# Kernel tuning notes

Measured on AMD Instinct MI355X. Metric: run time of the kernel, lower is better.

The kernel has to match this reference:

```python
import jax, jax.numpy as jnp
import numpy as np
import math

N, B, T, E = 4, 8, 2, 1024
H, D = 16, 64
S, L = 2048, 1024
NB = N * B

def setup_inputs() -> dict:
    key = jax.random.key(0)
    ks = jax.random.split(key, 10)
    sc = 0.02
    return {
        'hidden_states': jax.random.normal(ks[0], (NB, T, E), jnp.float32),
        'attention_mask': jnp.zeros((NB, 1, 1, S + L + T), jnp.float32),
        'past_prefix_key': jax.random.normal(ks[1], (N, H, S, D), jnp.float32),
        'past_prefix_value': jax.random.normal(ks[2], (N, H, S, D), jnp.float32),
        'past_key': jax.random.normal(ks[3], (NB, H, L, D), jnp.float32),
        'past_value': jax.random.normal(ks[4], (NB, H, L, D), jnp.float32),
        'Wq': jax.random.normal(ks[5], (E, E), jnp.float32) * sc,
        'bq': jnp.zeros((E,), jnp.float32),
        'Wk': jax.random.normal(ks[6], (E, E), jnp.float32) * sc,
        'bk': jnp.zeros((E,), jnp.float32),
        'Wv': jax.random.normal(ks[7], (E, E), jnp.float32) * sc,
        'bv': jnp.zeros((E,), jnp.float32),
    }

def _heads(x):
    # (NB, T, E) -> (NB, H, T, D)
    return x.reshape(NB, T, H, D).transpose(0, 2, 1, 3)

def reference(hidden_states, attention_mask, past_prefix_key, past_prefix_value,
              past_key, past_value, Wq, bq, Wk, bk, Wv, bv):
    scale = 1.0 / math.sqrt(D)
    q = _heads(hidden_states @ Wq.T + bq)   # (NB,H,T,D)
    k_new = _heads(hidden_states @ Wk.T + bk)
    v_new = _heads(hidden_states @ Wv.T + bv)

    # prefix scores: broadcast shared prefix KV across beams
    q_beam = q.reshape(N, B, H, T, D)
    prefix_scores = jnp.einsum('bxhtd,bhsd->bxhts', q_beam, past_prefix_key)
    prefix_scores = prefix_scores.reshape(NB, H, T, S) * scale

    # current KV = cached target prefix + new tokens
    k = jnp.concatenate([past_key, k_new], axis=2)   # (NB,H,L+T,D)
    v = jnp.concatenate([past_value, v_new], axis=2)
    cur_scores = jnp.einsum('bhtd,bhsd->bhts', q, k) * scale

    scores = jnp.concatenate([prefix_scores, cur_scores], axis=-1) + attention_mask
    probs = jax.nn.softmax(scores, axis=-1)          # (NB,H,T,S+L+T)

    prefix_probs = probs[..., :S].reshape(N, B, H, T, S)
    cur_probs = probs[..., S:]
    prefix_ctx = jnp.einsum('bxhts,bhsd->bxhtd', prefix_probs, past_prefix_value)
    prefix_ctx = prefix_ctx.reshape(NB, H, T, D)
    ctx = prefix_ctx + jnp.einsum('bhts,bhsd->bhtd', cur_probs, v)

    # (NB,H,T,D) -> (NB,T,E)
    return ctx.transpose(0, 2, 1, 3).reshape(NB, T, H * D)
```

## Files before the change

### kernel.cpp

```cpp
#include <hip/hip_runtime.h>
#include <hip/hip_bf16.h>

#define NB_  32
#define T_   2
#define E_   1024
#define H_   16
#define D_   64
#define S_   2048
#define L_   1024
#define TOT_ (S_ + L_ + T_)

#define PCH_  16
#define PLEN_ (S_ / PCH_)
#define NT_   8
#define CCH_  8
#define CLEN_ (L_ / CCH_)

#define PFXU_ (4 * H_ * PCH_)
#define CURU_ (NB_ * H_ * CCH_)

#define LOG2E_ 1.4426950408889634f
#define QS_ (0.125f * LOG2E_)

#define GLOAD_LDS16(g, l) __builtin_amdgcn_global_load_lds( \
    (const __attribute__((address_space(1))) void*)(g), \
    (__attribute__((address_space(3))) void*)(l), 16, 0, 0)

#define KEEP4(v) asm volatile("" : "+v"((v).x), "+v"((v).y), "+v"((v).z), "+v"((v).w))
#define KEEPF(a) asm volatile("" : "+v"(a))

__global__ __launch_bounds__(256) void qkv_kernel(
    const float* __restrict__ hidden,
    const float* __restrict__ Wq, const float* __restrict__ bq,
    const float* __restrict__ Wk, const float* __restrict__ bk,
    const float* __restrict__ Wv, const float* __restrict__ bv,
    float* __restrict__ qT,
    float* __restrict__ knew,
    float* __restrict__ vnew)
{
    __shared__ float ldsT[128 * 65];
    __shared__ float wlds[8 * 128];
    const int tid  = threadIdx.x;
    const int wave = tid >> 6;
    const int lane = tid & 63;
    const int eg0  = blockIdx.x * 8;
    const int mat  = eg0 >> 10;
    const int e0   = eg0 & 1023;
    int c0 = wave * 2;
    c0 = __builtin_amdgcn_readfirstlane(c0);

    const float* W    = (mat == 0) ? Wq : (mat == 1) ? Wk : Wv;
    const float* bias = (mat == 0) ? bq : (mat == 1) ? bk : bv;

    float aA0 = 0.f, aB0 = 0.f, aA1 = 0.f, aB1 = 0.f;

    for (int k0 = 0; k0 < 1024; k0 += 128) {
        __syncthreads();
        #pragma unroll
        for (int i = 0; i < 32; i++) {
            int f = i * 256 + tid;
            int r = f >> 7;
            int c = f & 127;
            ldsT[c * 65 + r] = hidden[r * 1024 + k0 + c];
        }
        {
            int wr = tid >> 5;
            int wc = (tid & 31) * 4;
            *reinterpret_cast<float4*>(&wlds[wr * 128 + wc]) =
                *reinterpret_cast<const float4*>(&W[(size_t)(e0 + wr) * 1024 + k0 + wc]);
        }
        __syncthreads();

        for (int kk = 0; kk < 128; kk += 4) {
            float h0 = ldsT[(kk + 0) * 65 + lane];
            float h1 = ldsT[(kk + 1) * 65 + lane];
            float h2 = ldsT[(kk + 2) * 65 + lane];
            float h3 = ldsT[(kk + 3) * 65 + lane];
            float4 w0 = *reinterpret_cast<const float4*>(&wlds[(c0 + 0) * 128 + kk]);
            float4 w1 = *reinterpret_cast<const float4*>(&wlds[(c0 + 1) * 128 + kk]);
            aA0 = fmaf(h0, w0.x, aA0); aA0 = fmaf(h1, w0.y, aA0);
            aB0 = fmaf(h2, w0.z, aB0); aB0 = fmaf(h3, w0.w, aB0);
            aA1 = fmaf(h0, w1.x, aA1); aA1 = fmaf(h1, w1.y, aA1);
            aB1 = fmaf(h2, w1.z, aB1); aB1 = fmaf(h3, w1.w, aB1);
        }
    }

    const int r = lane;
    #pragma unroll
    for (int j = 0; j < 2; j++) {
        int e_in = e0 + c0 + j;
        float val = ((j == 0) ? (aA0 + aB0) : (aA1 + aB1)) + bias[e_in];
        if (mat == 0) {
            qT[e_in * 64 + r] = val;
        } else {
            int nb = r >> 1, t = r & 1, h = e_in >> 6, d = e_in & 63;
            float* dst = (mat == 1) ? knew : vnew;
            dst[((nb * H_ + h) * T_ + t) * D_ + d] = val;
        }
    }
}

__global__ __launch_bounds__(256) void cur_partial_kernel(
    const float* __restrict__ mask,
    const float* __restrict__ pk,
    const float* __restrict__ pv,
    const float* __restrict__ qT,
    const float* __restrict__ knew,
    const float* __restrict__ vnew,
    float* __restrict__ cur_ctx,
    float* __restrict__ cur_l)
{
    __shared__ float smem[2080];
    const int tid = threadIdx.x;

    const int u     = blockIdx.x;
    const int b     = u >> 3;
    const int chunk = u & 7;
    const int nb    = b >> 4;
    const int h     = b & 15;
    const int g     = tid >> 4;
    const int l16   = tid & 15;
    const int d0    = l16 * 4;

    float qf0[4], qf1[4];
    #pragma unroll
    for (int j = 0; j < 4; j++) {
        const float* qb = qT + (h * 64 + d0 + j) * 64 + nb * 2;
        qf0[j] = qb[0] * QS_;
        qf1[j] = qb[1] * QS_;
    }

    const float* pk_b = pk + ((nb * H_ + h) * (size_t)L_) * D_;
    const float* pv_b = pv + ((nb * H_ + h) * (size_t)L_) * D_;
    const float* mrow = mask + nb * TOT_ + S_;
    const int p0 = chunk * CLEN_ + g;

    float mreg[8];
    #pragma unroll
    for (int i = 0; i < 8; i++) mreg[i] = mrow[p0 + i * 16] * LOG2E_;

    float4 kf[8], vf[8];
    #pragma unroll
    for (int i = 0; i < 8; i++) {
        kf[i] = *reinterpret_cast<const float4*>(pk_b + (size_t)(p0 + i * 16) * D_ + d0);
        vf[i] = *reinterpret_cast<const float4*>(pv_b + (size_t)(p0 + i * 16) * D_ + d0);
    }
    #pragma unroll
    for (int i = 0; i < 8; i++) { KEEP4(kf[i]); KEEP4(vf[i]); KEEPF(mreg[i]); }

    float l0 = 0.f, l1 = 0.f;
    float a0[4] = {0.f,0.f,0.f,0.f};
    float a1[4] = {0.f,0.f,0.f,0.f};

    #pragma unroll
    for (int i = 0; i < 8; i++) {
        float s0 = fmaf(qf0[0],kf[i].x, qf0[1]*kf[i].y) + fmaf(qf0[2],kf[i].z, qf0[3]*kf[i].w);
        float s1 = fmaf(qf1[0],kf[i].x, qf1[1]*kf[i].y) + fmaf(qf1[2],kf[i].z, qf1[3]*kf[i].w);
        #pragma unroll
        for (int off = 1; off < 16; off <<= 1) {
            s0 += __shfl_xor(s0, off, 64);
            s1 += __shfl_xor(s1, off, 64);
        }
        float e0 = exp2f(s0 + mreg[i]);
        float e1 = exp2f(s1 + mreg[i]);
        l0 += e0; l1 += e1;
        a0[0] += e0 * vf[i].x; a0[1] += e0 * vf[i].y; a0[2] += e0 * vf[i].z; a0[3] += e0 * vf[i].w;
        a1[0] += e1 * vf[i].x; a1[1] += e1 * vf[i].y; a1[2] += e1 * vf[i].z; a1[3] += e1 * vf[i].w;
    }

    if (chunk == 7 && g < 2) {
        const float* kn_b = knew + (nb * H_ + h) * (T_ * D_);
        const float* vn_b = vnew + (nb * H_ + h) * (T_ * D_);
        float4 kfn = *reinterpret_cast<const float4*>(kn_b + g * D_ + d0);
        float s0 = fmaf(qf0[0],kfn.x, qf0[1]*kfn.y) + fmaf(qf0[2],kfn.z, qf0[3]*kfn.w);
        float s1 = fmaf(qf1[0],kfn.x, qf1[1]*kfn.y) + fmaf(qf1[2],kfn.z, qf1[3]*kfn.w);
        #pragma unroll
        for (int off = 1; off < 16; off <<= 1) {
            s0 += __shfl_xor(s0, off, 64);
            s1 += __shfl_xor(s1, off, 64);
        }
        float mC = mrow[L_ + g] * LOG2E_;
        float e0 = exp2f(s0 + mC);
        float e1 = exp2f(s1 + mC);
        l0 += e0; l1 += e1;
        float4 vfn = *reinterpret_cast<const float4*>(vn_b + g * D_ + d0);
        a0[0] += e0 * vfn.x; a0[1] += e0 * vfn.y; a0[2] += e0 * vfn.z; a0[3] += e0 * vfn.w;
        a1[0] += e1 * vfn.x; a1[1] += e1 * vfn.y; a1[2] += e1 * vfn.z; a1[3] += e1 * vfn.w;
    }

    #pragma unroll
    for (int j = 0; j < 4; j++) {
        smem[g * 128 + d0 + j]      = a0[j];
        smem[g * 128 + 64 + d0 + j] = a1[j];
    }
    if (l16 == 0) { smem[2048 + g * 2] = l0; smem[2048 + g * 2 + 1] = l1; }
    __syncthreads();

    if (tid < 128) {
        int t = tid >> 6, d = tid & 63;
        float s = 0.f, l = 0.f;
        for (int g2 = 0; g2 < 16; g2++) {
            s += smem[g2 * 128 + t * 64 + d];
            l += smem[2048 + g2 * 2 + t];
        }
        cur_ctx[(u * 2 + t) * 64 + d] = s;
        if (d == 0) cur_l[u * 2 + t] = l;
    }
}

__global__ __launch_bounds__(256) void pfx_partial_kernel(
    const float* __restrict__ mask,
    const float* __restrict__ pfx_k,
    const float* __restrict__ pfx_v,
    const float* __restrict__ qT,
    float* __restrict__ pfx_ctx,
    float* __restrict__ pfx_l)
{
    __shared__ float smem[4160];
    const int tid = threadIdx.x;

    const int v     = blockIdx.x;
    const int n     = v >> 8;
    const int h     = (v >> 4) & 15;
    const int chunk = v & 15;
    const int wv    = tid >> 6;
    const int lane  = tid & 63;
    const int r     = lane & 15;
    const int c     = lane >> 4;

    float qreg[16];
    const float* qbase = qT + (h * 64 + c * 16) * 64 + (n * 16 + r);
    #pragma unroll
    for (int u = 0; u < 16; u++) qreg[u] = qbase[u * 64] * QS_;

    const size_t pos0 = (size_t)(n * H_ + h) * S_ + chunk * PLEN_;
    const float* kb = pfx_k + pos0 * D_;
    const float* vb = pfx_v + pos0 * D_;
    const float* mrow = mask + (n * 8 + (r >> 1)) * TOT_ + chunk * PLEN_;

    float ctx[16];
    #pragma unroll
    for (int u = 0; u < 16; u++) ctx[u] = 0.f;
    float lsum = 0.f;

    GLOAD_LDS16(kb + tid * 4, &smem[tid * 4]);
    GLOAD_LDS16(vb + tid * 4, &smem[1024 + tid * 4]);

    #pragma unroll 1
    for (int t = 0; t < NT_; t++) {
        const int bufo = (t & 1) * 2048;
        __syncthreads();

        float mreg[4];
        #pragma unroll
        for (int j = 0; j < 4; j++)
            mreg[j] = mrow[t * 16 + wv * 4 + j] * LOG2E_;

        if (t < NT_ - 1) {
            const int nbo = ((t + 1) & 1) * 2048;
            const float* kn = kb + (size_t)(t + 1) * 16 * 64;
            const float* vn = vb + (size_t)(t + 1) * 16 * 64;
            GLOAD_LDS16(kn + tid * 4, &smem[nbo + tid * 4]);
            GLOAD_LDS16(vn + tid * 4, &smem[nbo + 1024 + tid * 4]);
        }

        #pragma unroll
        for (int j = 0; j < 4; j++) {
            const int pp = wv * 4 + j;
            const float4* kq = reinterpret_cast<const float4*>(
                &smem[bufo + pp * 64 + c * 16]);
            float4 k0 = kq[0], k1 = kq[1], k2 = kq[2], k3 = kq[3];
            float sA = qreg[0]*k0.x;  sA = fmaf(qreg[1],k0.y,sA);
            sA = fmaf(qreg[2],k0.z,sA); sA = fmaf(qreg[3],k0.w,sA);
            float sB = qreg[4]*k1.x;  sB = fmaf(qreg[5],k1.y,sB);
            sB = fmaf(qreg[6],k1.z,sB); sB = fmaf(qreg[7],k1.w,sB);
            float sC = qreg[8]*k2.x;  sC = fmaf(qreg[9],k2.y,sC);
            sC = fmaf(qreg[10],k2.z,sC); sC = fmaf(qreg[11],k2.w,sC);
            float sD = qreg[12]*k3.x; sD = fmaf(qreg[13],k3.y,sD);
            sD = fmaf(qreg[14],k3.z,sD); sD = fmaf(qreg[15],k3.w,sD);
            float s = (sA + sB) + (sC + sD);
            s += __shfl_xor(s, 16, 64);
            s += __shfl_xor(s, 32, 64);
            float e = exp2f(s + mreg[j]);
            lsum += e;
            const float4* vq = reinterpret_cast<const float4*>(
                &smem[bufo + 1024 + pp * 64 + c * 16]);
            float4 v0 = vq[0], v1 = vq[1], v2 = vq[2], v3 = vq[3];
            ctx[0]  += e * v0.x; ctx[1]  += e * v0.y; ctx[2]  += e * v0.z; ctx[3]  += e * v0.w;
            ctx[4]  += e * v1.x; ctx[5]  += e * v1.y; ctx[6]  += e * v1.z; ctx[7]  += e * v1.w;
            ctx[8]  += e * v2.x; ctx[9]  += e * v2.y; ctx[10] += e * v2.z; ctx[11] += e * v2.w;
            ctx[12] += e * v3.x; ctx[13] += e * v3.y; ctx[14] += e * v3.z; ctx[15] += e * v3.w;
        }
    }

    __syncthreads();
    const int base = wv * 1024 + r * 64 + c * 16;
    #pragma unroll
    for (int u = 0; u < 16; u += 4)
        *reinterpret_cast<float4*>(&smem[base + u]) =
            make_float4(ctx[u], ctx[u+1], ctx[u+2], ctx[u+3]);
    if (c == 0) smem[4096 + wv * 16 + r] = lsum;
    __syncthreads();

    const int pc = (n * H_ + h) * PCH_ + chunk;
    for (int e = tid; e < 1024; e += 256) {
        float s = smem[e] + smem[1024 + e] + smem[2048 + e] + smem[3072 + e];
        pfx_ctx[pc * 1024 + e] = s;
    }
    if (tid < 16) {
        float l = smem[4096 + tid] + smem[4096 + 16 + tid]
                + smem[4096 + 32 + tid] + smem[4096 + 48 + tid];
        pfx_l[pc * 16 + tid] = l;
    }
}

__global__ __launch_bounds__(256) void combine_kernel(
    const float* __restrict__ cur_ctx, const float* __restrict__ cur_l,
    const float* __restrict__ pfx_ctx, const float* __restrict__ pfx_l,
    float* __restrict__ out)
{
    const int row = blockIdx.x >> 2;
    const int qtr = blockIdx.x & 3;
    const int nb  = row >> 1, t = row & 1;
    const int n   = nb >> 3;
    const int r   = (nb & 7) * 2 + t;
    const int e   = qtr * 256 + threadIdx.x;
    const int h   = e >> 6, d = e & 63;
    const int b   = nb * 16 + h;

    float val = 0.f, l = 0.f;
    #pragma unroll
    for (int ch = 0; ch < CCH_; ch++) {
        int cb = (b * CCH_ + ch);
        val += cur_ctx[(cb * 2 + t) * 64 + d];
        l   += cur_l[cb * 2 + t];
    }
    #pragma unroll
    for (int ch = 0; ch < PCH_; ch++) {
        int pc = (n * H_ + h) * PCH_ + ch;
        val += pfx_ctx[pc * 1024 + r * 64 + d];
        l   += pfx_l[pc * 16 + r];
    }
    out[row * 1024 + e] = val / l;
}

extern "C" void kernel_launch(void* const* d_in, const int* in_sizes, int n_in,
                              void* d_out, int out_size, void* d_ws, size_t ws_size,
                              hipStream_t stream) {
    const float* hidden = (const float*)d_in[0];
    const float* mask   = (const float*)d_in[1];
    const float* pfxk   = (const float*)d_in[2];
    const float* pfxv   = (const float*)d_in[3];
    const float* pk     = (const float*)d_in[4];
    const float* pv     = (const float*)d_in[5];
    const float* Wq     = (const float*)d_in[6];
    const float* bq     = (const float*)d_in[7];
    const float* Wk     = (const float*)d_in[8];
    const float* bk     = (const float*)d_in[9];
    const float* Wv     = (const float*)d_in[10];
    const float* bv     = (const float*)d_in[11];

    float* qT      = (float*)d_ws;
    float* knew    = qT + 65536;
    float* vnew    = knew + 65536;
    float* cur_ctx = vnew + 65536;
    float* cur_l   = cur_ctx + 524288;
    float* pfx_ctx = cur_l + 8192;
    float* pfx_l   = pfx_ctx + 1048576;

    qkv_kernel<<<384, 256, 0, stream>>>(hidden, Wq, bq, Wk, bk, Wv, bv,
                                        qT, knew, vnew);
    cur_partial_kernel<<<CURU_, 256, 0, stream>>>(
        mask, pk, pv, qT, knew, vnew, cur_ctx, cur_l);
    pfx_partial_kernel<<<PFXU_, 256, 0, stream>>>(
        mask, pfxk, pfxv, qT, pfx_ctx, pfx_l);
    combine_kernel<<<256, 256, 0, stream>>>(cur_ctx, cur_l, pfx_ctx, pfx_l,
                                            (float*)d_out);
}
```

Baseline: 107.2 us.

## Merge cur-attention chunks into one 1024-thread block per (beam, head)

Replaces the 4096 chunked 256-thread cur_partial blocks with 512 blocks of 1024 threads, each covering the full cached length plus the two new tokens for one (beam, head) in a strided loop. The new-token special case is folded into the main loop, and the chunk partials no longer go through global memory, so combine reads one value instead of eight. In exchange, the explicit register preloading of K/V (with asm keep barriers) is dropped in favour of one load per iteration. That may expose memory latency and lower the number of loads in flight on a bandwidth-bound stream, and the fewer, larger blocks can hurt occupancy.

```diff
diff --git a/kernel.cpp b/kernel.cpp
--- a/kernel.cpp
+++ b/kernel.cpp
@@ -13,11 +13,7 @@
 #define PCH_  16
 #define PLEN_ (S_ / PCH_)
 #define NT_   8
-#define CCH_  8
-#define CLEN_ (L_ / CCH_)
-
 #define PFXU_ (4 * H_ * PCH_)
-#define CURU_ (NB_ * H_ * CCH_)
 
 #define LOG2E_ 1.4426950408889634f
 #define QS_ (0.125f * LOG2E_)
@@ -25,9 +21,6 @@
 #define GLOAD_LDS16(g, l) __builtin_amdgcn_global_load_lds( \
     (const __attribute__((address_space(1))) void*)(g), \
     (__attribute__((address_space(3))) void*)(l), 16, 0, 0)
-
-#define KEEP4(v) asm volatile("" : "+v"((v).x), "+v"((v).y), "+v"((v).z), "+v"((v).w))
-#define KEEPF(a) asm volatile("" : "+v"(a))
 
 __global__ __launch_bounds__(256) void qkv_kernel(
     const float* __restrict__ hidden,
@@ -100,7 +93,7 @@
     }
 }
 
-__global__ __launch_bounds__(256) void cur_partial_kernel(
+__global__ __launch_bounds__(1024) void cur_kernel(
     const float* __restrict__ mask,
     const float* __restrict__ pk,
     const float* __restrict__ pv,
@@ -110,17 +103,17 @@
     float* __restrict__ cur_ctx,
     float* __restrict__ cur_l)
 {
-    __shared__ float smem[2080];
+    __shared__ float part_acc[64][128];
+    __shared__ float part_l[64][2];
+
+    const int bid = blockIdx.x;
+    const int nb  = bid >> 4;
+    const int h   = bid & 15;
+
     const int tid = threadIdx.x;
-
-    const int u     = blockIdx.x;
-    const int b     = u >> 3;
-    const int chunk = u & 7;
-    const int nb    = b >> 4;
-    const int h     = b & 15;
-    const int g     = tid >> 4;
-    const int l16   = tid & 15;
-    const int d0    = l16 * 4;
+    const int G   = tid >> 4;
+    const int l16 = tid & 15;
+    const int d0  = l16 * 4;
 
     float qf0[4], qf1[4];
     #pragma unroll
@@ -132,79 +125,55 @@
 
     const float* pk_b = pk + ((nb * H_ + h) * (size_t)L_) * D_;
     const float* pv_b = pv + ((nb * H_ + h) * (size_t)L_) * D_;
+    const float* kn_b = knew + (nb * H_ + h) * (T_ * D_);
+    const float* vn_b = vnew + (nb * H_ + h) * (T_ * D_);
     const float* mrow = mask + nb * TOT_ + S_;
-    const int p0 = chunk * CLEN_ + g;
-
-    float mreg[8];
-    #pragma unroll
-    for (int i = 0; i < 8; i++) mreg[i] = mrow[p0 + i * 16] * LOG2E_;
-
-    float4 kf[8], vf[8];
-    #pragma unroll
-    for (int i = 0; i < 8; i++) {
-        kf[i] = *reinterpret_cast<const float4*>(pk_b + (size_t)(p0 + i * 16) * D_ + d0);
-        vf[i] = *reinterpret_cast<const float4*>(pv_b + (size_t)(p0 + i * 16) * D_ + d0);
-    }
-    #pragma unroll
-    for (int i = 0; i < 8; i++) { KEEP4(kf[i]); KEEP4(vf[i]); KEEPF(mreg[i]); }
 
     float l0 = 0.f, l1 = 0.f;
-    float a0[4] = {0.f,0.f,0.f,0.f};
-    float a1[4] = {0.f,0.f,0.f,0.f};
-
-    #pragma unroll
-    for (int i = 0; i < 8; i++) {
-        float s0 = fmaf(qf0[0],kf[i].x, qf0[1]*kf[i].y) + fmaf(qf0[2],kf[i].z, qf0[3]*kf[i].w);
-        float s1 = fmaf(qf1[0],kf[i].x, qf1[1]*kf[i].y) + fmaf(qf1[2],kf[i].z, qf1[3]*kf[i].w);
+    float a0[4] = {0.f, 0.f, 0.f, 0.f};
+    float a1[4] = {0.f, 0.f, 0.f, 0.f};
+
+    for (int p = G; p < L_ + T_; p += 64) {
+        const float* kp;
+        const float* vp;
+        if (p < L_) { kp = pk_b + p * D_;        vp = pv_b + p * D_; }
+        else        { kp = kn_b + (p - L_) * D_; vp = vn_b + (p - L_) * D_; }
+
+        float4 kf = *reinterpret_cast<const float4*>(kp + d0);
+        float s0 = qf0[0] * kf.x + qf0[1] * kf.y + qf0[2] * kf.z + qf0[3] * kf.w;
+        float s1 = qf1[0] * kf.x + qf1[1] * kf.y + qf1[2] * kf.z + qf1[3] * kf.w;
         #pragma unroll
         for (int off = 1; off < 16; off <<= 1) {
             s0 += __shfl_xor(s0, off, 64);
             s1 += __shfl_xor(s1, off, 64);
         }
-        float e0 = exp2f(s0 + mreg[i]);
-        float e1 = exp2f(s1 + mreg[i]);
-        l0 += e0; l1 += e1;
-        a0[0] += e0 * vf[i].x; a0[1] += e0 * vf[i].y; a0[2] += e0 * vf[i].z; a0[3] += e0 * vf[i].w;
-        a1[0] += e1 * vf[i].x; a1[1] += e1 * vf[i].y; a1[2] += e1 * vf[i].z; a1[3] += e1 * vf[i].w;
-    }
-
-    if (chunk == 7 && g < 2) {
-        const float* kn_b = knew + (nb * H_ + h) * (T_ * D_);
-        const float* vn_b = vnew + (nb * H_ + h) * (T_ * D_);
-        float4 kfn = *reinterpret_cast<const float4*>(kn_b + g * D_ + d0);
-        float s0 = fmaf(qf0[0],kfn.x, qf0[1]*kfn.y) + fmaf(qf0[2],kfn.z, qf0[3]*kfn.w);
-        float s1 = fmaf(qf1[0],kfn.x, qf1[1]*kfn.y) + fmaf(qf1[2],kfn.z, qf1[3]*kfn.w);
-        #pragma unroll
-        for (int off = 1; off < 16; off <<= 1) {
-            s0 += __shfl_xor(s0, off, 64);
-            s1 += __shfl_xor(s1, off, 64);
-        }
-        float mC = mrow[L_ + g] * LOG2E_;
+        float mC = mrow[p] * LOG2E_;
         float e0 = exp2f(s0 + mC);
         float e1 = exp2f(s1 + mC);
-        l0 += e0; l1 += e1;
-        float4 vfn = *reinterpret_cast<const float4*>(vn_b + g * D_ + d0);
-        a0[0] += e0 * vfn.x; a0[1] += e0 * vfn.y; a0[2] += e0 * vfn.z; a0[3] += e0 * vfn.w;
-        a1[0] += e1 * vfn.x; a1[1] += e1 * vfn.y; a1[2] += e1 * vfn.z; a1[3] += e1 * vfn.w;
-    }
-
+        l0 += e0;
+        l1 += e1;
+        float4 vf = *reinterpret_cast<const float4*>(vp + d0);
+        a0[0] += e0 * vf.x; a0[1] += e0 * vf.y; a0[2] += e0 * vf.z; a0[3] += e0 * vf.w;
+        a1[0] += e1 * vf.x; a1[1] += e1 * vf.y; a1[2] += e1 * vf.z; a1[3] += e1 * vf.w;
+    }
+
+    if (l16 == 0) { part_l[G][0] = l0; part_l[G][1] = l1; }
     #pragma unroll
     for (int j = 0; j < 4; j++) {
-        smem[g * 128 + d0 + j]      = a0[j];
-        smem[g * 128 + 64 + d0 + j] = a1[j];
-    }
-    if (l16 == 0) { smem[2048 + g * 2] = l0; smem[2048 + g * 2 + 1] = l1; }
+        part_acc[G][d0 + j]      = a0[j];
+        part_acc[G][64 + d0 + j] = a1[j];
+    }
     __syncthreads();
 
     if (tid < 128) {
         int t = tid >> 6, d = tid & 63;
         float s = 0.f, l = 0.f;
-        for (int g2 = 0; g2 < 16; g2++) {
-            s += smem[g2 * 128 + t * 64 + d];
-            l += smem[2048 + g2 * 2 + t];
-        }
-        cur_ctx[(u * 2 + t) * 64 + d] = s;
-        if (d == 0) cur_l[u * 2 + t] = l;
+        for (int g = 0; g < 64; g++) {
+            s += part_acc[g][t * 64 + d];
+            l += part_l[g][t];
+        }
+        cur_ctx[(bid * 2 + t) * 64 + d] = s;
+        if (d == 0) cur_l[bid * 2 + t] = l;
     }
 }
 
@@ -328,13 +297,8 @@
     const int h   = e >> 6, d = e & 63;
     const int b   = nb * 16 + h;
 
-    float val = 0.f, l = 0.f;
-    #pragma unroll
-    for (int ch = 0; ch < CCH_; ch++) {
-        int cb = (b * CCH_ + ch);
-        val += cur_ctx[(cb * 2 + t) * 64 + d];
-        l   += cur_l[cb * 2 + t];
-    }
+    float val = cur_ctx[(b * 2 + t) * 64 + d];
+    float l   = cur_l[b * 2 + t];
     #pragma unroll
     for (int ch = 0; ch < PCH_; ch++) {
         int pc = (n * H_ + h) * PCH_ + ch;
@@ -364,13 +328,13 @@
     float* knew    = qT + 65536;
     float* vnew    = knew + 65536;
     float* cur_ctx = vnew + 65536;
-    float* cur_l   = cur_ctx + 524288;
-    float* pfx_ctx = cur_l + 8192;
+    float* cur_l   = cur_ctx + 65536;
+    float* pfx_ctx = cur_l + 1024;
     float* pfx_l   = pfx_ctx + 1048576;
 
     qkv_kernel<<<384, 256, 0, stream>>>(hidden, Wq, bq, Wk, bk, Wv, bv,
                                         qT, knew, vnew);
-    cur_partial_kernel<<<CURU_, 256, 0, stream>>>(
+    cur_kernel<<<512, 1024, 0, stream>>>(
         mask, pk, pv, qT, knew, vnew, cur_ctx, cur_l);
     pfx_partial_kernel<<<PFXU_, 256, 0, stream>>>(
         mask, pfxk, pfxv, qT, pfx_ctx, pfx_l);
```

New measurement: 111.6 us. 4.0% more time.
